# Optimization experiments

Hardware: AMD Instinct MI355X
Metric: run time of the kernel (lower is better)

Reference implementation:

```python
import jax, jax.numpy as jnp
import numpy as np

B, H, W, C = 64, 56, 56, 96
HEADS, WIN, SHIFT = 3, 7, 3
HD = C // HEADS          # head dim = 32
MLP_H = 4 * C            # mlp_ratio = 4
NW = (H // WIN) * (W // WIN)  # 64 windows per image
WW = WIN * WIN           # 49 tokens per window


def _rel_index():
    ch, cw = np.meshgrid(np.arange(WIN), np.arange(WIN), indexing='ij')
    coords = np.stack([ch, cw]).reshape(2, -1)            # [2, 49]
    rel = (coords[:, :, None] - coords[:, None, :]).transpose(1, 2, 0)
    rel[..., 0] += WIN - 1
    rel[..., 1] += WIN - 1
    rel[..., 0] *= 2 * WIN - 1
    return rel.sum(-1)                                    # [49, 49] int

REL_IDX = _rel_index()


def _attn_mask():
    # shifted-window mask per the original Swin implementation
    img = np.zeros((H, W))
    cnt = 0
    for hs in (slice(0, -WIN), slice(-WIN, -SHIFT), slice(-SHIFT, None)):
        for ws in (slice(0, -WIN), slice(-WIN, -SHIFT), slice(-SHIFT, None)):
            img[hs, ws] = cnt
            cnt += 1
    mw = img.reshape(H // WIN, WIN, W // WIN, WIN).transpose(0, 2, 1, 3).reshape(-1, WW)
    m = mw[:, None, :] - mw[:, :, None]
    return np.where(m != 0, -100.0, 0.0).astype(np.float32)  # [NW, 49, 49]

ATTN_MASK = jnp.asarray(_attn_mask())


def window_partition(x):
    # [B, H, W, C] -> [B*NW, 49, C]
    x = x.reshape(-1, H // WIN, WIN, W // WIN, WIN, C)
    return x.transpose(0, 1, 3, 2, 4, 5).reshape(-1, WW, C)


def window_reverse(w):
    # [B*NW, 49, C] -> [B, H, W, C]
    w = w.reshape(-1, H // WIN, W // WIN, WIN, WIN, C)
    return w.transpose(0, 1, 3, 2, 4, 5).reshape(-1, H, W, C)


def layernorm(x, w, b):
    mu = x.mean(-1, keepdims=True)
    var = ((x - mu) ** 2).mean(-1, keepdims=True)
    return (x - mu) / jnp.sqrt(var + 1e-5) * w + b


def setup_inputs() -> dict:
    key = jax.random.key(0)
    ks = jax.random.split(key, 16)
    s = 0.02
    return {
        'x': jax.random.normal(ks[0], (B, H * W, C), jnp.float32),
        'norm1_w': jnp.ones((C,), jnp.float32),
        'norm1_b': jnp.zeros((C,), jnp.float32),
        'qkv_w': jax.random.normal(ks[1], (3 * C, C), jnp.float32) * s,
        'qkv_b': jnp.zeros((3 * C,), jnp.float32),
        'rel_bias': jax.random.normal(ks[2], ((2 * WIN - 1) ** 2, HEADS), jnp.float32) * s,
        'proj_w': jax.random.normal(ks[3], (C, C), jnp.float32) * s,
        'proj_b': jnp.zeros((C,), jnp.float32),
        'norm2_w': jnp.ones((C,), jnp.float32),
        'norm2_b': jnp.zeros((C,), jnp.float32),
        'fc1_w': jax.random.normal(ks[4], (MLP_H, C), jnp.float32) * s,
        'fc1_b': jnp.zeros((MLP_H,), jnp.float32),
        'fc2_w': jax.random.normal(ks[5], (C, MLP_H), jnp.float32) * s,
        'fc2_b': jnp.zeros((C,), jnp.float32),
    }


def reference(x, norm1_w, norm1_b, qkv_w, qkv_b, rel_bias, proj_w, proj_b,
              norm2_w, norm2_b, fc1_w, fc1_b, fc2_w, fc2_b):
    shortcut = x
    h = layernorm(x, norm1_w, norm1_b).reshape(B, H, W, C)
    # cyclic shift (SW-MSA)
    h = jnp.roll(h, (-SHIFT, -SHIFT), axis=(1, 2))
    xw = window_partition(h)                               # [B*NW, 49, C]
    qkv = (xw @ qkv_w.T + qkv_b).reshape(-1, WW, 3, HEADS, HD)
    qkv = qkv.transpose(2, 0, 3, 1, 4)                     # [3, B*NW, heads, 49, hd]
    q, k, v = qkv[0], qkv[1], qkv[2]
    attn = jnp.einsum('whqd,whkd->whqk', q * (HD ** -0.5), k)   # [B*NW, heads, 49, 49]
    attn = attn + rel_bias[REL_IDX].transpose(2, 0, 1)[None]
    attn = attn.reshape(B, NW, HEADS, WW, WW) + ATTN_MASK[None, :, None]
    attn = jax.nn.softmax(attn.reshape(-1, HEADS, WW, WW), axis=-1)
    out = jnp.einsum('whqk,whkd->whqd', attn, v)
    out = out.transpose(0, 2, 1, 3).reshape(-1, WW, C)
    out = out @ proj_w.T + proj_b
    h = window_reverse(out)
    h = jnp.roll(h, (SHIFT, SHIFT), axis=(1, 2)).reshape(B, H * W, C)
    x = shortcut + h
    h2 = layernorm(x, norm2_w, norm2_b)
    h2 = jax.nn.gelu(h2 @ fc1_w.T + fc1_b, approximate=False) @ fc2_w.T + fc2_b
    return x + h2
```

## Files before the change

### kernel.cpp

```cpp
#include <hip/hip_runtime.h>
#include <hip/hip_bf16.h>
#include <math.h>

#define BATCH 64
#define HH 56
#define CH 96
#define HEADS 3
#define WIN 7
#define SHIFT 3
#define TOK 49
#define MLPH 384
#define SCALE 0.17677669529663687f

typedef short bf16x8 __attribute__((ext_vector_type(8)));
typedef float f32x4 __attribute__((ext_vector_type(4)));

#define MFMA(a, b, c) __builtin_amdgcn_mfma_f32_16x16x32_bf16((a), (b), (c), 0, 0, 0)
#define MEMFENCE() asm volatile("" ::: "memory")

__device__ __forceinline__ bf16x8 ldfrag(const __hip_bfloat16* p) {
    return *(const bf16x8*)p;
}
__device__ __forceinline__ unsigned short f2bf(float f) {
    __hip_bfloat16 h = __float2bfloat16(f);
    unsigned short u; __builtin_memcpy(&u, &h, 2); return u;
}

__global__ __launch_bounds__(256) void prep(
    const float* __restrict__ qkvw, const float* __restrict__ projw,
    const float* __restrict__ fc1w, const float* __restrict__ fc2w,
    const float* __restrict__ relb,
    __hip_bfloat16* __restrict__ wbf, float* __restrict__ btab)
{
    int i = blockIdx.x * 256 + threadIdx.x;
    if (i < 27648)        wbf[i] = __float2bfloat16(qkvw[i]);
    else if (i < 36864)   wbf[i] = __float2bfloat16(projw[i - 27648]);
    else if (i < 73728)   wbf[i] = __float2bfloat16(fc1w[i - 36864]);
    else if (i < 110592)  wbf[i] = __float2bfloat16(fc2w[i - 73728]);
    else {
        int j = i - 110592;
        int cat = j / 12288;
        int r = j - cat * 12288;
        int h = r >> 12;
        int r2 = r & 4095;
        int q = r2 >> 6, k = r2 & 63;
        float v;
        if (k >= TOK) v = -10000.f;
        else if (q >= TOK) v = 0.f;
        else {
            int qi = q / WIN, qj = q - qi * WIN;
            int ki = k / WIN, kj = k - ki * WIN;
            int ridx = (qi - ki + 6) * 13 + (qj - kj + 6);
            v = relb[ridx * HEADS + h];
            int rqh = (cat & 2) ? (qi < 4 ? 1 : 2) : 0;
            int rqw = (cat & 1) ? (qj < 4 ? 1 : 2) : 0;
            int rkh = (cat & 2) ? (ki < 4 ? 1 : 2) : 0;
            int rkw = (cat & 1) ? (kj < 4 ? 1 : 2) : 0;
            if (rqh * 3 + rqw != rkh * 3 + rkw) v -= 100.f;
        }
        btab[j] = v;
    }
}

__global__ __launch_bounds__(256) void swin_fused(
    const float* __restrict__ x,
    const float* __restrict__ n1w, const float* __restrict__ n1b,
    const __hip_bfloat16* __restrict__ wqkv, const float* __restrict__ qkvb,
    const float* __restrict__ btab,
    const __hip_bfloat16* __restrict__ wproj, const float* __restrict__ projb,
    const float* __restrict__ n2w, const float* __restrict__ n2b,
    const __hip_bfloat16* __restrict__ w1, const float* __restrict__ b1,
    const __hip_bfloat16* __restrict__ w2, const float* __restrict__ b2,
    float* __restrict__ out)
{
    __shared__ __align__(16) char arena[65536];
    auto XL   = (__hip_bfloat16(*)[104])(arena);
    auto Qf   = (__hip_bfloat16(*)[104])(arena + 13312);
    auto Kf   = (__hip_bfloat16(*)[104])(arena + 26624);
    auto Vt   = (__hip_bfloat16(*)[72])(arena + 39936);
    auto Pw   = (__hip_bfloat16(*)[16][72])(arena + 53760);
    auto resL = (float(*)[104])(arena + 13312);
    auto Hs   = (__hip_bfloat16(*)[200])(arena + 39936);

    const int blk = blockIdx.x;
    const int b = blk >> 6, win = blk & 63;
    const int wi = win >> 3, wj = win & 7;
    const int cat = ((wi == 7) << 1) | (wj == 7);
    const int tid = threadIdx.x;
    const int lane = tid & 63, w = tid >> 6;
    const int lr = lane & 15, g = lane >> 4;
    const int k0 = g * 8;
    const size_t bbase = (size_t)b * (HH * HH * CH);

    {
        int r = tid >> 2, p = tid & 3;
        if (r < TOK) {
            int ti = r / WIN, tj = r - (r / WIN) * WIN;
            int ph = wi * WIN + ti + SHIFT; if (ph >= HH) ph -= HH;
            int pw = wj * WIN + tj + SHIFT; if (pw >= HH) pw -= HH;
            const float4* xr = (const float4*)(x + bbase + (size_t)(ph * HH + pw) * CH + p * 24);
            float v[24]; float s = 0.f, s2 = 0.f;
            #pragma unroll
            for (int i = 0; i < 6; ++i) {
                float4 f = xr[i];
                v[4*i] = f.x; v[4*i+1] = f.y; v[4*i+2] = f.z; v[4*i+3] = f.w;
            }
            #pragma unroll
            for (int i = 0; i < 24; ++i) { s += v[i]; s2 += v[i] * v[i]; }
            s  += __shfl_xor(s, 1);  s  += __shfl_xor(s, 2);
            s2 += __shfl_xor(s2, 1); s2 += __shfl_xor(s2, 2);
            float mu = s * (1.f / CH);
            float rstd = rsqrtf(s2 * (1.f / CH) - mu * mu + 1e-5f);
            #pragma unroll
            for (int i = 0; i < 24; ++i) {
                int c = p * 24 + i;
                XL[r][c] = __float2bfloat16((v[i] - mu) * rstd * n1w[c] + n1b[c]);
            }
        } else {
            #pragma unroll
            for (int i = 0; i < 24; ++i) XL[r][p * 24 + i] = __float2bfloat16(0.f);
        }
    }
    __syncthreads();

    {
        bf16x8 Bx[4][3];
        #pragma unroll
        for (int tt = 0; tt < 4; ++tt)
            #pragma unroll
            for (int ks = 0; ks < 3; ++ks)
                Bx[tt][ks] = ldfrag(&XL[tt * 16 + lr][ks * 32 + k0]);
        #pragma unroll
        for (int nn = 0; nn < 5; ++nn) {
            int n = w + 4 * nn;
            if (n < 18) {
                const __hip_bfloat16* wp = wqkv + (n * 16 + lr) * CH + k0;
                bf16x8 Af[3];
                #pragma unroll
                for (int ks = 0; ks < 3; ++ks) Af[ks] = ldfrag(wp + ks * 32);
                f32x4 acc[4];
                #pragma unroll
                for (int tt = 0; tt < 4; ++tt) acc[tt] = (f32x4){0.f, 0.f, 0.f, 0.f};
                #pragma unroll
                for (int ks = 0; ks < 3; ++ks)
                    #pragma unroll
                    for (int tt = 0; tt < 4; ++tt)
                        acc[tt] = MFMA(Af[ks], Bx[tt][ks], acc[tt]);
                f32x4 b4 = *(const f32x4*)(qkvb + n * 16 + 4 * g);
                #pragma unroll
                for (int tt = 0; tt < 4; ++tt) {
                    int tokr = tt * 16 + lr;
                    if (n < 6) {
                        ushort4 u;
                        u.x = f2bf((acc[tt][0] + b4[0]) * SCALE);
                        u.y = f2bf((acc[tt][1] + b4[1]) * SCALE);
                        u.z = f2bf((acc[tt][2] + b4[2]) * SCALE);
                        u.w = f2bf((acc[tt][3] + b4[3]) * SCALE);
                        *(ushort4*)&Qf[tokr][n * 16 + 4 * g] = u;
                    } else if (n < 12) {
                        ushort4 u;
                        u.x = f2bf(acc[tt][0] + b4[0]);
                        u.y = f2bf(acc[tt][1] + b4[1]);
                        u.z = f2bf(acc[tt][2] + b4[2]);
                        u.w = f2bf(acc[tt][3] + b4[3]);
                        *(ushort4*)&Kf[tokr][(n - 6) * 16 + 4 * g] = u;
                    } else {
                        #pragma unroll
                        for (int j = 0; j < 4; ++j)
                            Vt[(n - 12) * 16 + 4 * g + j][tokr] =
                                __float2bfloat16(acc[tt][j] + b4[j]);
                    }
                }
            }
        }
    }
    __syncthreads();

    for (int u = w; u < 12; u += 4) {
        int h = u >> 2, qt = u & 3;
        bf16x8 qfrag = ldfrag(&Qf[qt * 16 + lr][h * 32 + k0]);
        f32x4 s[4];
        #pragma unroll
        for (int kt = 0; kt < 4; ++kt) {
            f32x4 z = {0.f, 0.f, 0.f, 0.f};
            s[kt] = MFMA(ldfrag(&Kf[kt * 16 + lr][h * 32 + k0]), qfrag, z);
        }
        const float* bt = btab + (((cat * HEADS + h) << 12) | ((qt * 16 + lr) << 6));
        #pragma unroll
        for (int kt = 0; kt < 4; ++kt)
            s[kt] += *(const f32x4*)(bt + kt * 16 + 4 * g);
        float m = -1e30f;
        #pragma unroll
        for (int kt = 0; kt < 4; ++kt)
            #pragma unroll
            for (int j = 0; j < 4; ++j) m = fmaxf(m, s[kt][j]);
        m = fmaxf(m, __shfl_xor(m, 16));
        m = fmaxf(m, __shfl_xor(m, 32));
        float e[4][4]; float sum = 0.f;
        #pragma unroll
        for (int kt = 0; kt < 4; ++kt)
            #pragma unroll
            for (int j = 0; j < 4; ++j) { e[kt][j] = __expf(s[kt][j] - m); sum += e[kt][j]; }
        sum += __shfl_xor(sum, 16);
        sum += __shfl_xor(sum, 32);
        float inv = 1.f / sum;
        #pragma unroll
        for (int kt = 0; kt < 4; ++kt) {
            ushort2 p0, p1;
            p0.x = f2bf(e[kt][0] * inv); p0.y = f2bf(e[kt][1] * inv);
            p1.x = f2bf(e[kt][2] * inv); p1.y = f2bf(e[kt][3] * inv);
            *(ushort2*)&Pw[w][lr][kt * 16 + g * 4]     = p0;
            *(ushort2*)&Pw[w][lr][kt * 16 + g * 4 + 2] = p1;
        }
        MEMFENCE();
        #pragma unroll
        for (int dt = 0; dt < 2; ++dt) {
            f32x4 o = {0.f, 0.f, 0.f, 0.f};
            #pragma unroll
            for (int ks = 0; ks < 2; ++ks) {
                bf16x8 pa = ldfrag(&Pw[w][lr][ks * 32 + k0]);
                bf16x8 vb = ldfrag(&Vt[h * 32 + dt * 16 + lr][ks * 32 + k0]);
                o = MFMA(pa, vb, o);
            }
            #pragma unroll
            for (int j = 0; j < 4; ++j)
                XL[qt * 16 + g * 4 + j][h * 32 + dt * 16 + lr] = __float2bfloat16(o[j]);
        }
    }
    __syncthreads();

    {
        bf16x8 Bx[4][3];
        #pragma unroll
        for (int tt = 0; tt < 4; ++tt)
            #pragma unroll
            for (int ks = 0; ks < 3; ++ks)
                Bx[tt][ks] = ldfrag(&XL[tt * 16 + lr][ks * 32 + k0]);
        #pragma unroll
        for (int nn = 0; nn < 2; ++nn) {
            int n = w + 4 * nn;
            if (n < 6) {
                const __hip_bfloat16* wp = wproj + (n * 16 + lr) * CH + k0;
                bf16x8 Af[3];
                #pragma unroll
                for (int ks = 0; ks < 3; ++ks) Af[ks] = ldfrag(wp + ks * 32);
                f32x4 acc[4];
                #pragma unroll
                for (int tt = 0; tt < 4; ++tt) acc[tt] = (f32x4){0.f, 0.f, 0.f, 0.f};
                #pragma unroll
                for (int ks = 0; ks < 3; ++ks)
                    #pragma unroll
                    for (int tt = 0; tt < 4; ++tt)
                        acc[tt] = MFMA(Af[ks], Bx[tt][ks], acc[tt]);
                f32x4 b4 = *(const f32x4*)(projb + n * 16 + 4 * g);
                #pragma unroll
                for (int tt = 0; tt < 4; ++tt) {
                    int tokr = tt * 16 + lr;
                    if (tokr < TOK) {
                        int ti = tokr / WIN, tj = tokr - (tokr / WIN) * WIN;
                        int ph = wi * WIN + ti + SHIFT; if (ph >= HH) ph -= HH;
                        int pw = wj * WIN + tj + SHIFT; if (pw >= HH) pw -= HH;
                        size_t gi = bbase + (size_t)(ph * HH + pw) * CH + n * 16 + 4 * g;
                        f32x4 x4 = *(const f32x4*)(x + gi);
                        *(f32x4*)&resL[tokr][n * 16 + 4 * g] = x4 + acc[tt] + b4;
                    } else {
                        *(f32x4*)&resL[tokr][n * 16 + 4 * g] = (f32x4){0.f, 0.f, 0.f, 0.f};
                    }
                }
            }
        }
    }
    __syncthreads();

    {
        int r = tid >> 2, p = tid & 3;
        float v[24]; float s = 0.f, s2 = 0.f;
        #pragma unroll
        for (int i = 0; i < 6; ++i) {
            f32x4 f = *(const f32x4*)&resL[r][p * 24 + 4 * i];
            v[4*i] = f[0]; v[4*i+1] = f[1]; v[4*i+2] = f[2]; v[4*i+3] = f[3];
        }
        #pragma unroll
        for (int i = 0; i < 24; ++i) { s += v[i]; s2 += v[i] * v[i]; }
        s  += __shfl_xor(s, 1);  s  += __shfl_xor(s, 2);
        s2 += __shfl_xor(s2, 1); s2 += __shfl_xor(s2, 2);
        float mu = s * (1.f / CH);
        float rstd = rsqrtf(s2 * (1.f / CH) - mu * mu + 1e-5f);
        #pragma unroll
        for (int i = 0; i < 6; ++i) {
            const float* wp4 = n2w + p * 24 + 4 * i;
            const float* bp4 = n2b + p * 24 + 4 * i;
            ushort4 u;
            u.x = f2bf((v[4*i]   - mu) * rstd * wp4[0] + bp4[0]);
            u.y = f2bf((v[4*i+1] - mu) * rstd * wp4[1] + bp4[1]);
            u.z = f2bf((v[4*i+2] - mu) * rstd * wp4[2] + bp4[2]);
            u.w = f2bf((v[4*i+3] - mu) * rstd * wp4[3] + bp4[3]);
            *(ushort4*)&XL[r][p * 24 + 4 * i] = u;
        }
    }
    __syncthreads();

    const int mh = w & 1, nh = w >> 1;
    f32x4 acc2[3][2];
    #pragma unroll
    for (int nt = 0; nt < 3; ++nt)
        #pragma unroll
        for (int mi = 0; mi < 2; ++mi) acc2[nt][mi] = (f32x4){0.f, 0.f, 0.f, 0.f};

    #pragma unroll
    for (int c = 0; c < 2; ++c) {
        bf16x8 Bx[4][3];
        #pragma unroll
        for (int tt = 0; tt < 4; ++tt)
            #pragma unroll
            for (int ks = 0; ks < 3; ++ks)
                Bx[tt][ks] = ldfrag(&XL[tt * 16 + lr][ks * 32 + k0]);

        #pragma unroll
        for (int nn = 0; nn < 3; ++nn) {
            int nl = w + 4 * nn;
            int ncol = c * 192 + nl * 16;
            const __hip_bfloat16* wp = w1 + (ncol + lr) * CH + k0;
            bf16x8 Af[3];
            #pragma unroll
            for (int ks = 0; ks < 3; ++ks) Af[ks] = ldfrag(wp + ks * 32);
            f32x4 acc[4];
            #pragma unroll
            for (int tt = 0; tt < 4; ++tt) acc[tt] = (f32x4){0.f, 0.f, 0.f, 0.f};
            #pragma unroll
            for (int ks = 0; ks < 3; ++ks)
                #pragma unroll
                for (int tt = 0; tt < 4; ++tt)
                    acc[tt] = MFMA(Af[ks], Bx[tt][ks], acc[tt]);
            f32x4 b4 = *(const f32x4*)(b1 + ncol + 4 * g);
            #pragma unroll
            for (int tt = 0; tt < 4; ++tt) {
                ushort4 u;
                #pragma unroll
                for (int j = 0; j < 4; ++j) {
                    float v = acc[tt][j] + b4[j];
                    float ge = v / (1.f + __expf(-1.702f * v));
                    ((unsigned short*)&u)[j] = f2bf(ge);
                }
                *(ushort4*)&Hs[tt * 16 + lr][nl * 16 + 4 * g] = u;
            }
        }
        __syncthreads();

        #pragma unroll
        for (int k = 0; k < 6; ++k) {
            bf16x8 h0 = ldfrag(&Hs[mh * 32 + lr][k * 32 + k0]);
            bf16x8 h1 = ldfrag(&Hs[mh * 32 + 16 + lr][k * 32 + k0]);
            #pragma unroll
            for (int nt = 0; nt < 3; ++nt) {
                bf16x8 Af = ldfrag(w2 + (nh * 48 + nt * 16 + lr) * MLPH + c * 192 + k * 32 + k0);
                acc2[nt][0] = MFMA(Af, h0, acc2[nt][0]);
                acc2[nt][1] = MFMA(Af, h1, acc2[nt][1]);
            }
        }
        __syncthreads();
    }

    #pragma unroll
    for (int nt = 0; nt < 3; ++nt) {
        f32x4 b4 = *(const f32x4*)(b2 + nh * 48 + nt * 16 + 4 * g);
        #pragma unroll
        for (int mi = 0; mi < 2; ++mi) {
            int tokr = mh * 32 + mi * 16 + lr;
            if (tokr < TOK) {
                int ti = tokr / WIN, tj = tokr - (tokr / WIN) * WIN;
                int ph = wi * WIN + ti + SHIFT; if (ph >= HH) ph -= HH;
                int pw = wj * WIN + tj + SHIFT; if (pw >= HH) pw -= HH;
                size_t gi = bbase + (size_t)(ph * HH + pw) * CH + nh * 48 + nt * 16 + 4 * g;
                f32x4 r4 = *(const f32x4*)&resL[tokr][nh * 48 + nt * 16 + 4 * g];
                *(f32x4*)(out + gi) = r4 + acc2[nt][mi] + b4;
            }
        }
    }
}

extern "C" void kernel_launch(void* const* d_in, const int* in_sizes, int n_in,
                              void* d_out, int out_size, void* d_ws, size_t ws_size,
                              hipStream_t stream) {
    const float* x     = (const float*)d_in[0];
    const float* n1w   = (const float*)d_in[1];
    const float* n1b   = (const float*)d_in[2];
    const float* qkvw  = (const float*)d_in[3];
    const float* qkvb  = (const float*)d_in[4];
    const float* relb  = (const float*)d_in[5];
    const float* projw = (const float*)d_in[6];
    const float* projb = (const float*)d_in[7];
    const float* n2w   = (const float*)d_in[8];
    const float* n2b   = (const float*)d_in[9];
    const float* fc1w  = (const float*)d_in[10];
    const float* fc1b  = (const float*)d_in[11];
    const float* fc2w  = (const float*)d_in[12];
    const float* fc2b  = (const float*)d_in[13];
    float* out = (float*)d_out;

    __hip_bfloat16* wbf = (__hip_bfloat16*)d_ws;
    float* btab = (float*)((char*)d_ws + 221184);
    const __hip_bfloat16* wqkv  = wbf;
    const __hip_bfloat16* wproj = wbf + 27648;
    const __hip_bfloat16* wfc1  = wbf + 36864;
    const __hip_bfloat16* wfc2  = wbf + 73728;

    prep<<<624, 256, 0, stream>>>(qkvw, projw, fc1w, fc2w, relb, wbf, btab);
    swin_fused<<<BATCH * 64, 256, 0, stream>>>(
        x, n1w, n1b, wqkv, qkvb, btab, wproj, projb,
        n2w, n2b, wfc1, fc1b, wfc2, fc2b, out);
}
```

Baseline: 219.4 us.

## Shrink LDS arena and fuse proj residual with LN2 in registers

Cuts the shared-memory arena from 64KB to about 48.5KB so three blocks can sit on a CU, and declares that with launch bounds. To free the space, Q is written over the LN1 buffer, and the residual is kept in registers instead of in an LDS fp32 buffer. The projection GEMM is re-tiled so each wave owns 32 tokens by 48 channels, and LN2 uses per-wave partial sums exchanged through a tiny LDS buffer. The risks are extra register pressure under the 3-block bound and an added barrier after the QKV fragment loads.

```diff
diff --git a/kernel.cpp b/kernel.cpp
--- a/kernel.cpp
+++ b/kernel.cpp
@@ -62,7 +62,12 @@
     }
 }
 
-__global__ __launch_bounds__(256) void swin_fused(
+#define OFF_KF 13312
+#define OFF_VT 26624
+#define OFF_PW 40448
+#define ARENA_BYTES 49664
+
+__global__ __launch_bounds__(256, 3) void swin_fused(
     const float* __restrict__ x,
     const float* __restrict__ n1w, const float* __restrict__ n1b,
     const __hip_bfloat16* __restrict__ wqkv, const float* __restrict__ qkvb,
@@ -73,14 +78,13 @@
     const __hip_bfloat16* __restrict__ w2, const float* __restrict__ b2,
     float* __restrict__ out)
 {
-    __shared__ __align__(16) char arena[65536];
+    __shared__ __align__(16) char arena[ARENA_BYTES];
     auto XL   = (__hip_bfloat16(*)[104])(arena);
-    auto Qf   = (__hip_bfloat16(*)[104])(arena + 13312);
-    auto Kf   = (__hip_bfloat16(*)[104])(arena + 26624);
-    auto Vt   = (__hip_bfloat16(*)[72])(arena + 39936);
-    auto Pw   = (__hip_bfloat16(*)[16][72])(arena + 53760);
-    auto resL = (float(*)[104])(arena + 13312);
-    auto Hs   = (__hip_bfloat16(*)[200])(arena + 39936);
+    auto Kf   = (__hip_bfloat16(*)[104])(arena + OFF_KF);
+    auto Vt   = (__hip_bfloat16(*)[72])(arena + OFF_VT);
+    auto Pw   = (__hip_bfloat16(*)[16][72])(arena + OFF_PW);
+    auto Hs   = (__hip_bfloat16(*)[200])(arena + OFF_KF);
+    auto part = (float(*)[2][2])(arena + OFF_PW);
 
     const int blk = blockIdx.x;
     const int b = blk >> 6, win = blk & 63;
@@ -130,6 +134,8 @@
             #pragma unroll
             for (int ks = 0; ks < 3; ++ks)
                 Bx[tt][ks] = ldfrag(&XL[tt * 16 + lr][ks * 32 + k0]);
+        __syncthreads();
+
         #pragma unroll
         for (int nn = 0; nn < 5; ++nn) {
             int n = w + 4 * nn;
@@ -156,7 +162,7 @@
                         u.y = f2bf((acc[tt][1] + b4[1]) * SCALE);
                         u.z = f2bf((acc[tt][2] + b4[2]) * SCALE);
                         u.w = f2bf((acc[tt][3] + b4[3]) * SCALE);
-                        *(ushort4*)&Qf[tokr][n * 16 + 4 * g] = u;
+                        *(ushort4*)&XL[tokr][n * 16 + 4 * g] = u;
                     } else if (n < 12) {
                         ushort4 u;
                         u.x = f2bf(acc[tt][0] + b4[0]);
@@ -178,7 +184,7 @@
 
     for (int u = w; u < 12; u += 4) {
         int h = u >> 2, qt = u & 3;
-        bf16x8 qfrag = ldfrag(&Qf[qt * 16 + lr][h * 32 + k0]);
+        bf16x8 qfrag = ldfrag(&XL[qt * 16 + lr][h * 32 + k0]);
         f32x4 s[4];
         #pragma unroll
         for (int kt = 0; kt < 4; ++kt) {
@@ -226,81 +232,99 @@
             for (int j = 0; j < 4; ++j)
                 XL[qt * 16 + g * 4 + j][h * 32 + dt * 16 + lr] = __float2bfloat16(o[j]);
         }
+        MEMFENCE();
     }
     __syncthreads();
 
+    const int mh = w & 1, nh = w >> 1;
+    size_t rowoff[2];
+    int tokv[2];
+    #pragma unroll
+    for (int mi = 0; mi < 2; ++mi) {
+        int tokr = mh * 32 + mi * 16 + lr;
+        tokv[mi] = tokr;
+        int ti = tokr / WIN, tj = tokr - (tokr / WIN) * WIN;
+        int ph = wi * WIN + ti + SHIFT; if (ph >= HH) ph -= HH;
+        int pw = wj * WIN + tj + SHIFT; if (pw >= HH) pw -= HH;
+        rowoff[mi] = bbase + (size_t)(ph * HH + pw) * CH;
+    }
+    f32x4 res[3][2];
     {
-        bf16x8 Bx[4][3];
-        #pragma unroll
-        for (int tt = 0; tt < 4; ++tt)
+        bf16x8 Bx2[2][3];
+        #pragma unroll
+        for (int mi = 0; mi < 2; ++mi)
             #pragma unroll
             for (int ks = 0; ks < 3; ++ks)
-                Bx[tt][ks] = ldfrag(&XL[tt * 16 + lr][ks * 32 + k0]);
-        #pragma unroll
-        for (int nn = 0; nn < 2; ++nn) {
-            int n = w + 4 * nn;
-            if (n < 6) {
-                const __hip_bfloat16* wp = wproj + (n * 16 + lr) * CH + k0;
-                bf16x8 Af[3];
-                #pragma unroll
-                for (int ks = 0; ks < 3; ++ks) Af[ks] = ldfrag(wp + ks * 32);
-                f32x4 acc[4];
-                #pragma unroll
-                for (int tt = 0; tt < 4; ++tt) acc[tt] = (f32x4){0.f, 0.f, 0.f, 0.f};
-                #pragma unroll
-                for (int ks = 0; ks < 3; ++ks)
-                    #pragma unroll
-                    for (int tt = 0; tt < 4; ++tt)
-                        acc[tt] = MFMA(Af[ks], Bx[tt][ks], acc[tt]);
-                f32x4 b4 = *(const f32x4*)(projb + n * 16 + 4 * g);
-                #pragma unroll
-                for (int tt = 0; tt < 4; ++tt) {
-                    int tokr = tt * 16 + lr;
-                    if (tokr < TOK) {
-                        int ti = tokr / WIN, tj = tokr - (tokr / WIN) * WIN;
-                        int ph = wi * WIN + ti + SHIFT; if (ph >= HH) ph -= HH;
-                        int pw = wj * WIN + tj + SHIFT; if (pw >= HH) pw -= HH;
-                        size_t gi = bbase + (size_t)(ph * HH + pw) * CH + n * 16 + 4 * g;
-                        f32x4 x4 = *(const f32x4*)(x + gi);
-                        *(f32x4*)&resL[tokr][n * 16 + 4 * g] = x4 + acc[tt] + b4;
-                    } else {
-                        *(f32x4*)&resL[tokr][n * 16 + 4 * g] = (f32x4){0.f, 0.f, 0.f, 0.f};
-                    }
+                Bx2[mi][ks] = ldfrag(&XL[(mh * 2 + mi) * 16 + lr][ks * 32 + k0]);
+        #pragma unroll
+        for (int nt = 0; nt < 3; ++nt) {
+            int ch0 = nh * 48 + nt * 16;
+            const __hip_bfloat16* wp = wproj + (ch0 + lr) * CH + k0;
+            bf16x8 Af[3];
+            #pragma unroll
+            for (int ks = 0; ks < 3; ++ks) Af[ks] = ldfrag(wp + ks * 32);
+            f32x4 acc[2];
+            acc[0] = (f32x4){0.f, 0.f, 0.f, 0.f};
+            acc[1] = (f32x4){0.f, 0.f, 0.f, 0.f};
+            #pragma unroll
+            for (int ks = 0; ks < 3; ++ks) {
+                acc[0] = MFMA(Af[ks], Bx2[0][ks], acc[0]);
+                acc[1] = MFMA(Af[ks], Bx2[1][ks], acc[1]);
+            }
+            f32x4 pb4 = *(const f32x4*)(projb + ch0 + 4 * g);
+            #pragma unroll
+            for (int mi = 0; mi < 2; ++mi) {
+                f32x4 x4 = *(const f32x4*)(x + rowoff[mi] + ch0 + 4 * g);
+                res[nt][mi] = acc[mi] + pb4 + x4;
+            }
+        }
+    }
+
+    {
+        float s[2] = {0.f, 0.f}, s2[2] = {0.f, 0.f};
+        #pragma unroll
+        for (int mi = 0; mi < 2; ++mi)
+            #pragma unroll
+            for (int nt = 0; nt < 3; ++nt)
+                #pragma unroll
+                for (int j = 0; j < 4; ++j) {
+                    float v = res[nt][mi][j];
+                    s[mi] += v; s2[mi] += v * v;
                 }
-            }
+        #pragma unroll
+        for (int mi = 0; mi < 2; ++mi) {
+            s[mi]  += __shfl_xor(s[mi], 16);  s[mi]  += __shfl_xor(s[mi], 32);
+            s2[mi] += __shfl_xor(s2[mi], 16); s2[mi] += __shfl_xor(s2[mi], 32);
+            part[tokv[mi]][nh][0] = s[mi];
+            part[tokv[mi]][nh][1] = s2[mi];
         }
     }
     __syncthreads();
-
-    {
-        int r = tid >> 2, p = tid & 3;
-        float v[24]; float s = 0.f, s2 = 0.f;
-        #pragma unroll
-        for (int i = 0; i < 6; ++i) {
-            f32x4 f = *(const f32x4*)&resL[r][p * 24 + 4 * i];
-            v[4*i] = f[0]; v[4*i+1] = f[1]; v[4*i+2] = f[2]; v[4*i+3] = f[3];
-        }
-        #pragma unroll
-        for (int i = 0; i < 24; ++i) { s += v[i]; s2 += v[i] * v[i]; }
-        s  += __shfl_xor(s, 1);  s  += __shfl_xor(s, 2);
-        s2 += __shfl_xor(s2, 1); s2 += __shfl_xor(s2, 2);
-        float mu = s * (1.f / CH);
-        float rstd = rsqrtf(s2 * (1.f / CH) - mu * mu + 1e-5f);
-        #pragma unroll
-        for (int i = 0; i < 6; ++i) {
-            const float* wp4 = n2w + p * 24 + 4 * i;
-            const float* bp4 = n2b + p * 24 + 4 * i;
+    float mu[2], rstd[2];
+    #pragma unroll
+    for (int mi = 0; mi < 2; ++mi) {
+        float ts  = part[tokv[mi]][0][0] + part[tokv[mi]][1][0];
+        float ts2 = part[tokv[mi]][0][1] + part[tokv[mi]][1][1];
+        mu[mi] = ts * (1.f / CH);
+        rstd[mi] = rsqrtf(ts2 * (1.f / CH) - mu[mi] * mu[mi] + 1e-5f);
+    }
+    #pragma unroll
+    for (int nt = 0; nt < 3; ++nt) {
+        int ch0 = nh * 48 + nt * 16 + 4 * g;
+        f32x4 w4 = *(const f32x4*)(n2w + ch0);
+        f32x4 b4 = *(const f32x4*)(n2b + ch0);
+        #pragma unroll
+        for (int mi = 0; mi < 2; ++mi) {
             ushort4 u;
-            u.x = f2bf((v[4*i]   - mu) * rstd * wp4[0] + bp4[0]);
-            u.y = f2bf((v[4*i+1] - mu) * rstd * wp4[1] + bp4[1]);
-            u.z = f2bf((v[4*i+2] - mu) * rstd * wp4[2] + bp4[2]);
-            u.w = f2bf((v[4*i+3] - mu) * rstd * wp4[3] + bp4[3]);
-            *(ushort4*)&XL[r][p * 24 + 4 * i] = u;
+            #pragma unroll
+            for (int j = 0; j < 4; ++j)
+                ((unsigned short*)&u)[j] =
+                    f2bf((res[nt][mi][j] - mu[mi]) * rstd[mi] * w4[j] + b4[j]);
+            *(ushort4*)&XL[tokv[mi]][ch0] = u;
         }
     }
     __syncthreads();
 
-    const int mh = w & 1, nh = w >> 1;
     f32x4 acc2[3][2];
     #pragma unroll
     for (int nt = 0; nt < 3; ++nt)
@@ -366,14 +390,9 @@
         f32x4 b4 = *(const f32x4*)(b2 + nh * 48 + nt * 16 + 4 * g);
         #pragma unroll
         for (int mi = 0; mi < 2; ++mi) {
-            int tokr = mh * 32 + mi * 16 + lr;
-            if (tokr < TOK) {
-                int ti = tokr / WIN, tj = tokr - (tokr / WIN) * WIN;
-                int ph = wi * WIN + ti + SHIFT; if (ph >= HH) ph -= HH;
-                int pw = wj * WIN + tj + SHIFT; if (pw >= HH) pw -= HH;
-                size_t gi = bbase + (size_t)(ph * HH + pw) * CH + nh * 48 + nt * 16 + 4 * g;
-                f32x4 r4 = *(const f32x4*)&resL[tokr][nh * 48 + nt * 16 + 4 * g];
-                *(f32x4*)(out + gi) = r4 + acc2[nt][mi] + b4;
+            if (tokv[mi] < TOK) {
+                size_t gi = rowoff[mi] + nh * 48 + nt * 16 + 4 * g;
+                *(f32x4*)(out + gi) = res[nt][mi] + acc2[nt][mi] + b4;
             }
         }
     }
```

New measurement: 197.6 us. -9.9%, faster.
